# Kernel optimization log

Hardware: AMD Instinct MI355X
Metric: run time of the kernel (lower is better)

Reference implementation:

```python
import jax, jax.numpy as jnp
import numpy as np

B, N, D_MODEL, H = 2, 512, 256, 8
DH, DS, DE = 8, 8, 8          # hyperbolic / spherical / euclidean component dims
HEAD = D_MODEL // H           # 32
HALF = HEAD // 2              # 16 rope frequencies
KAPPA_S = 1.0                 # spherical curvature
EPS = 1e-6


def setup_inputs() -> dict:
    key = jax.random.key(0)
    ks = jax.random.split(key, 10)
    h = jax.random.normal(ks[0], (B, N, D_MODEL), jnp.float32)
    # manifold coords: hyperbolic part inside Poincare ball, spherical part on unit sphere
    xh = 0.3 * jnp.tanh(jax.random.normal(ks[1], (B, N, DH), jnp.float32))
    xs_raw = jax.random.normal(ks[2], (B, N, DS), jnp.float32)
    xs = xs_raw / jnp.linalg.norm(xs_raw, axis=-1, keepdims=True)
    xe = jax.random.normal(ks[3], (B, N, DE), jnp.float32)
    x = jnp.concatenate([xh, xs, xe], axis=-1)
    def lin(k):
        return 0.05 * jax.random.normal(k, (D_MODEL, D_MODEL), jnp.float32)
    inp = dict(
        h=h, x=x,
        Wq=lin(ks[4]), bq=jnp.zeros((D_MODEL,), jnp.float32),
        Wk=lin(ks[5]), bk=jnp.zeros((D_MODEL,), jnp.float32),
        Wv=lin(ks[6]), bv=jnp.zeros((D_MODEL,), jnp.float32),
        Wo=lin(ks[7]), bo=jnp.zeros((D_MODEL,), jnp.float32),
        w_kernel=jnp.ones((H, 3), jnp.float32),   # torch init: ones(num_heads, num_comp)
        beta=jnp.ones((H,), jnp.float32),
        edge_bias=0.1 * jax.random.normal(ks[8], (B, 1, N, N), jnp.float32),
        node_mask=jnp.ones((B, N), bool),
    )
    return inp


def _pairwise_geometry(x):
    """Returns dh (B,N,N), sdot (B,N,N), de2 (B,N,N), dist (B,N,N)."""
    xh, xs, xe = x[..., :DH], x[..., DH:DH + DS], x[..., DH + DS:]
    # hyperbolic: Poincare-ball distance arccosh(1 + 2|a-b|^2 / ((1-|a|^2)(1-|b|^2)))
    dh2_num = jnp.sum((xh[:, :, None, :] - xh[:, None, :, :]) ** 2, -1)
    one_m = 1.0 - jnp.sum(xh * xh, -1)                               # (B,N)
    arg = 1.0 + 2.0 * dh2_num / (one_m[:, :, None] * one_m[:, None, :])
    dh = jnp.arccosh(jnp.maximum(arg, 1.0 + EPS))
    # spherical: arccos of dot (unit vectors); raw dot kept for the kernel term
    sdot = jnp.einsum('bnd,bmd->bnm', xs, xs)
    ds = jnp.arccos(jnp.clip(sdot, -1.0 + EPS, 1.0 - EPS)) / np.sqrt(KAPPA_S)
    # euclidean: squared distance (kernel uses -d^2; product dist uses d^2)
    de2 = jnp.sum((xe[:, :, None, :] - xe[:, None, :, :]) ** 2, -1)
    dist = jnp.sqrt(dh * dh + ds * ds + de2)
    return dh, sdot, de2, dist


def reference(h, x, Wq, bq, Wk, bk, Wv, bv, Wo, bo, w_kernel, beta, edge_bias, node_mask):
    scale = 1.0 / np.sqrt(HEAD)
    rope_freq = jnp.exp(-np.log(10000.0) * jnp.arange(HALF, dtype=jnp.float32) / HALF)

    def heads(t):  # (B,N,D) -> (B,H,N,head)
        return t.reshape(B, N, H, HEAD).transpose(0, 2, 1, 3)

    Q = heads(h @ Wq.T + bq)
    K = heads(h @ Wk.T + bk)
    V = heads(h @ Wv.T + bv)

    dh, sdot, de2, dist = _pairwise_geometry(x)

    # M-RoPE: rotate Q by pairwise angle theta_ij = omega * d_M(x_i, x_j)
    theta = dist[..., None] * rope_freq                  # (B,N,N,half)
    cos_t = jnp.cos(theta)[:, None]                      # (B,1,N,N,half)
    sin_t = jnp.sin(theta)[:, None]
    q1, q2 = Q[..., 0::2], Q[..., 1::2]                  # (B,H,N,half)
    k1, k2 = K[..., 0::2], K[..., 1::2]
    qk_same = q1[:, :, :, None, :] * k1[:, :, None, :, :] + q2[:, :, :, None, :] * k2[:, :, None, :, :]
    qk_cross = q1[:, :, :, None, :] * k2[:, :, None, :, :] - q2[:, :, :, None, :] * k1[:, :, None, :, :]
    attn = (cos_t * qk_same + sin_t * qk_cross).sum(-1) * scale   # (B,H,N,N)

    # geodesic kernel bias: per-component kernels [H:-d_H, S:k*a.b, E:-|a-b|^2]
    kernel_stack = jnp.stack([-dh, KAPPA_S * sdot, -de2], axis=-1)  # (B,N,N,3)
    geo = jnp.einsum('hc,bnmc->bhnm', w_kernel, kernel_stack)
    attn = attn + beta[None, :, None, None] * geo + edge_bias

    attn = jnp.where(node_mask[:, None, None, :], attn, -jnp.inf)
    p = jax.nn.softmax(attn, axis=-1)
    out = jnp.einsum('bhnm,bhmd->bhnd', p, V).transpose(0, 2, 1, 3).reshape(B, N, D_MODEL)
    return out @ Wo.T + bo
```

## Files before the change

kernel.cpp:

```cpp
#include <hip/hip_runtime.h>

#define N_TOK 512
#define NH 8

typedef __attribute__((ext_vector_type(8))) short short8;
typedef __attribute__((ext_vector_type(4))) short short4v;
typedef __attribute__((ext_vector_type(4))) float f32x4;
typedef __attribute__((ext_vector_type(2))) _Float16 half2v;
typedef __attribute__((ext_vector_type(4))) _Float16 half4v;
typedef __attribute__((ext_vector_type(8))) _Float16 half8v;

__device__ __forceinline__ unsigned short f2bf(float f) {
    union { float f; unsigned u; } v; v.f = f;
    return (unsigned short)((v.u + 0x7FFF + ((v.u >> 16) & 1)) >> 16);
}

__global__ __launch_bounds__(256) void gemm_qkv_mfma(
    const float* __restrict__ A, const float* __restrict__ x,
    const float* __restrict__ Wq, const float* __restrict__ Wk, const float* __restrict__ Wv,
    const float* __restrict__ bq, const float* __restrict__ bk, const float* __restrict__ bv,
    float* __restrict__ Qb, _Float16* __restrict__ KT2, float* __restrict__ Vb,
    float* __restrict__ xT)
{
    const int bx = blockIdx.x;
    const int t = threadIdx.x;
    if (bx >= 768) {
        int idx = bx - 768;
        int b = idx / 24, k = idx % 24;
        const float* src = x + (size_t)b * 512 * 24 + k;
        float* dst = xT + (size_t)b * 12288 + k * 512;
        for (int j = t; j < 512; j += 256) dst[j] = src[j * 24];
        return;
    }
    const int z = bx >> 8, rem = bx & 255;
    const int m0 = (rem >> 3) * 32, n0 = (rem & 7) * 32;
    const float* W    = (z == 0) ? Wq : (z == 1) ? Wk : Wv;
    const float* bias = (z == 0) ? bq : (z == 1) ? bk : bv;

    __shared__ short As[32][264];
    __shared__ short Ws[32][264];

    #pragma unroll
    for (int r = 0; r < 8; ++r) {
        int idx = t + 256 * r;
        int row = idx >> 6, c4 = (idx & 63) * 4;
        float4 a = *(const float4*)&A[(m0 + row) * 256 + c4];
        short4v pa = {(short)f2bf(a.x), (short)f2bf(a.y), (short)f2bf(a.z), (short)f2bf(a.w)};
        *(short4v*)&As[row][c4] = pa;
        float4 w = *(const float4*)&W[(n0 + row) * 256 + c4];
        short4v pw = {(short)f2bf(w.x), (short)f2bf(w.y), (short)f2bf(w.z), (short)f2bf(w.w)};
        *(short4v*)&Ws[row][c4] = pw;
    }
    __syncthreads();

    const int w = t >> 6, lane = t & 63;
    const int wm = (w >> 1) * 16, wn = (w & 1) * 16;
    const int frow = lane & 15, kq = lane >> 4;

    f32x4 acc = {0.f, 0.f, 0.f, 0.f};
    #pragma unroll
    for (int k0 = 0; k0 < 8; ++k0) {
        short8 af = *(const short8*)&As[wm + frow][k0 * 32 + kq * 8];
        short8 wf = *(const short8*)&Ws[wn + frow][k0 * 32 + kq * 8];
        if (z == 1) acc = __builtin_amdgcn_mfma_f32_16x16x32_bf16(wf, af, acc, 0, 0, 0);
        else        acc = __builtin_amdgcn_mfma_f32_16x16x32_bf16(af, wf, acc, 0, 0, 0);
    }
    const int col = lane & 15, rq = (lane >> 4) * 4;
    if (z == 1) {
        int tok = m0 + wm + col;
        int bb = tok >> 9, jloc = tok & 511;
        #pragma unroll
        for (int r = 0; r < 4; ++r) {
            int d = n0 + wn + rq + r;
            KT2[(size_t)bb * 131072 + (size_t)(d >> 1) * 1024 + jloc * 2 + (d & 1)]
                = (_Float16)(acc[r] + bias[d]);
        }
    } else {
        float* C = (z == 0) ? Qb : Vb;
        const float sc = (z == 0) ? 0.17677669529663687f : 1.0f;
        float bsv = bias[n0 + wn + col];
        #pragma unroll
        for (int r = 0; r < 4; ++r)
            C[(m0 + wm + rq + r) * 256 + n0 + wn + col] = (acc[r] + bsv) * sc;
    }
}

__global__ __launch_bounds__(512, 4) void attn_kernel(
    const float* __restrict__ Q, const _Float16* __restrict__ KT2, const float* __restrict__ V,
    const float* __restrict__ x, const float* __restrict__ xT,
    const float* __restrict__ wker, const float* __restrict__ beta,
    const float* __restrict__ eb, float* __restrict__ Ao)
{
    const int i0 = blockIdx.x * 2;
    const int b  = blockIdx.y;
    const int t  = threadIdx.x;
    const int lane = t & 63;
    const int h = __builtin_amdgcn_readfirstlane(t >> 6);

    __shared__ half8v csn[16][2][64];
    __shared__ float es[2][NH][128];
    __shared__ float gdh[2][512], gsd[2][512], gde[2][512], gdist[2][512];

    {
        const float* xc = xT + (size_t)b * 12288 + t;
        float xv[24];
        #pragma unroll
        for (int k = 0; k < 24; ++k) xv[k] = xc[k * 512];
        float oj = 0.f;
        #pragma unroll
        for (int k = 0; k < 8; ++k) oj += xv[k] * xv[k];
        #pragma unroll
        for (int p = 0; p < 2; ++p) {
            const float* xi = x + (size_t)(b * N_TOK + i0 + p) * 24;
            float onemi = 1.0f, dh2 = 0.f, sd = 0.f, de2 = 0.f;
            #pragma unroll
            for (int k = 0; k < 8; ++k) {
                onemi -= xi[k] * xi[k];
                float d = xi[k] - xv[k]; dh2 += d * d;
            }
            #pragma unroll
            for (int k = 0; k < 8; ++k) sd += xi[8 + k] * xv[8 + k];
            #pragma unroll
            for (int k = 0; k < 8; ++k) { float d = xi[16 + k] - xv[16 + k]; de2 += d * d; }
            float arg = fmaf(2.0f * dh2, __builtin_amdgcn_rcpf(onemi * (1.0f - oj)), 1.0f);
            arg = fmaxf(arg, 1.0f + 1e-6f);
            float dh = __logf(arg + __builtin_amdgcn_sqrtf(fmaf(arg, arg, -1.0f)));
            float sdc = fminf(fmaxf(sd, -1.0f + 1e-6f), 1.0f - 1e-6f);
            float ax = fabsf(sdc);
            float pp = fmaf(ax, -0.0012624911f, 0.0066700901f);
            pp = fmaf(pp, ax, -0.0170881256f);
            pp = fmaf(pp, ax,  0.0308918810f);
            pp = fmaf(pp, ax, -0.0501743046f);
            pp = fmaf(pp, ax,  0.0889789874f);
            pp = fmaf(pp, ax, -0.2145988016f);
            pp = fmaf(pp, ax,  1.5707963050f);
            pp *= __builtin_amdgcn_sqrtf(1.0f - ax);
            float dsp = (sdc < 0.f) ? (3.14159265358979f - pp) : pp;
            float dist = __builtin_amdgcn_sqrtf(fmaf(dh, dh, fmaf(dsp, dsp, de2)));
            gdh[p][t] = dh; gsd[p][t] = sd; gde[p][t] = de2; gdist[p][t] = dist;
        }
    }

    const float* q0p = Q + (size_t)(b * N_TOK + i0) * 256 + h * 32;
    const float* q1p = q0p + 256;
    const float bet = beta[h];
    const float bw0 = bet * wker[h * 3 + 0], bw1 = bet * wker[h * 3 + 1], bw2 = bet * wker[h * 3 + 2];

    const int gjj = t & 127;
    const int gfh = __builtin_amdgcn_readfirstlane((t >> 7) & 1);
    const int gii = __builtin_amdgcn_readfirstlane(t >> 8);
    float frq[8];
    #pragma unroll
    for (int r = 0; r < 8; ++r)
        frq[r] = __expf(-0.5756462732485115f * (float)(gfh * 8 + r));

    float dsum[2] = {0.f, 0.f};
    float accv[2][4] = {{0.f,0.f,0.f,0.f},{0.f,0.f,0.f,0.f}};
    const int jsub = lane >> 3, dq = lane & 7;

    auto build = [&](int tile) {
        float d = gdist[gii][tile * 128 + gjj];
        #pragma unroll
        for (int r = 0; r < 8; ++r) {
            float sv, cv;
            __sincosf(d * frq[r], &sv, &cv);
            half4v p;
            p[0] = (_Float16)cv; p[1] = (_Float16)sv;
            p[2] = (_Float16)(-sv); p[3] = (_Float16)cv;
            ((half4v*)&csn[gfh * 8 + r][gii][gjj >> 1])[gjj & 1] = p;
        }
    };

    __syncthreads();
    build(0);
    const float* ebp0 = eb + ((size_t)b * N_TOK + i0) * N_TOK + 2 * lane;
    const float* ebp1 = ebp0 + N_TOK;
    float2 ebn0 = *(const float2*)ebp0;
    float2 ebn1 = *(const float2*)ebp1;
    __syncthreads();

    const _Float16* kbase = KT2 + (size_t)b * 131072 + (size_t)(h * 16) * 1024 + 4 * lane;

    for (int tile = 0; tile < 4; ++tile) {
        float2 eb0 = ebn0, eb1 = ebn1;
        if (tile < 3) {
            ebn0 = *(const float2*)(ebp0 + (tile + 1) * 128);
            ebn1 = *(const float2*)(ebp1 + (tile + 1) * 128);
        }
        {
            const _Float16* kp = kbase + tile * 256;
            half4v karr[16];
            #pragma unroll
            for (int f = 0; f < 16; ++f) karr[f] = *(const half4v*)(kp + f * 1024);

            float dot[2][2] = {{0.f, 0.f}, {0.f, 0.f}};
            #pragma unroll
            for (int f = 0; f < 16; ++f) {
                half2v k0 = {karr[f][0], karr[f][1]};
                half2v k1 = {karr[f][2], karr[f][3]};
                float q10 = q0p[2 * f], q20 = q0p[2 * f + 1];
                float q11 = q1p[2 * f], q21 = q1p[2 * f + 1];
                #pragma unroll
                for (int ii = 0; ii < 2; ++ii) {
                    half8v c8 = csn[f][ii][lane];
                    half2v cs0 = {c8[0], c8[1]}, rt0 = {c8[2], c8[3]};
                    half2v cs1 = {c8[4], c8[5]}, rt1 = {c8[6], c8[7]};
#if __has_builtin(__builtin_amdgcn_fdot2)
                    float u0 = __builtin_amdgcn_fdot2(cs0, k0, 0.f, false);
                    float v0 = __builtin_amdgcn_fdot2(rt0, k0, 0.f, false);
                    float u1 = __builtin_amdgcn_fdot2(cs1, k1, 0.f, false);
                    float v1 = __builtin_amdgcn_fdot2(rt1, k1, 0.f, false);
#else
                    float u0 = (float)cs0[0]*(float)k0[0] + (float)cs0[1]*(float)k0[1];
                    float v0 = (float)rt0[0]*(float)k0[0] + (float)rt0[1]*(float)k0[1];
                    float u1 = (float)cs1[0]*(float)k1[0] + (float)cs1[1]*(float)k1[1];
                    float v1 = (float)rt1[0]*(float)k1[0] + (float)rt1[1]*(float)k1[1];
#endif
                    float qa = ii ? q11 : q10, qb = ii ? q21 : q20;
                    dot[ii][0] = fmaf(qa, u0, fmaf(qb, v0, dot[ii][0]));
                    dot[ii][1] = fmaf(qa, u1, fmaf(qb, v1, dot[ii][1]));
                }
            }
            #pragma unroll
            for (int ii = 0; ii < 2; ++ii) {
                float2 g1 = *(const float2*)&gdh[ii][tile * 128 + 2 * lane];
                float2 g2 = *(const float2*)&gsd[ii][tile * 128 + 2 * lane];
                float2 g3 = *(const float2*)&gde[ii][tile * 128 + 2 * lane];
                float2 e2 = ii ? eb1 : eb0;
                float s0 = dot[ii][0] + (bw1 * g2.x - bw0 * g1.x - bw2 * g3.x) + e2.x;
                float s1 = dot[ii][1] + (bw1 * g2.y - bw0 * g1.y - bw2 * g3.y) + e2.y;
                float e0 = __expf(s0), e1 = __expf(s1);
                dsum[ii] += e0 + e1;
                *(float2*)&es[ii][h][2 * lane] = make_float2(e0, e1);
            }
        }
        if (tile < 3) { __syncthreads(); build(tile + 1); }
        {
            const float* vp = V + (size_t)(b * N_TOK + tile * 128 + jsub) * 256 + h * 32 + dq * 4;
            #pragma unroll
            for (int it = 0; it < 16; ++it) {
                float4 v4 = *(const float4*)(vp + it * 8 * 256);
                float e0 = es[0][h][it * 8 + jsub], e1 = es[1][h][it * 8 + jsub];
                accv[0][0] += e0 * v4.x; accv[0][1] += e0 * v4.y;
                accv[0][2] += e0 * v4.z; accv[0][3] += e0 * v4.w;
                accv[1][0] += e1 * v4.x; accv[1][1] += e1 * v4.y;
                accv[1][2] += e1 * v4.z; accv[1][3] += e1 * v4.w;
            }
        }
        if (tile < 3) __syncthreads();
    }

    #pragma unroll
    for (int ii = 0; ii < 2; ++ii) {
        float v = dsum[ii];
        v += __shfl_xor(v, 1);  v += __shfl_xor(v, 2);  v += __shfl_xor(v, 4);
        v += __shfl_xor(v, 8);  v += __shfl_xor(v, 16); v += __shfl_xor(v, 32);
        dsum[ii] = 1.0f / v;
    }
    #pragma unroll
    for (int ii = 0; ii < 2; ++ii)
        #pragma unroll
        for (int dd = 0; dd < 4; ++dd) {
            float a = accv[ii][dd];
            a += __shfl_xor(a, 8); a += __shfl_xor(a, 16); a += __shfl_xor(a, 32);
            accv[ii][dd] = a;
        }
    if (jsub == 0) {
        #pragma unroll
        for (int ii = 0; ii < 2; ++ii) {
            float4 o;
            o.x = accv[ii][0] * dsum[ii]; o.y = accv[ii][1] * dsum[ii];
            o.z = accv[ii][2] * dsum[ii]; o.w = accv[ii][3] * dsum[ii];
            *(float4*)&Ao[(size_t)(b * N_TOK + i0 + ii) * 256 + h * 32 + dq * 4] = o;
        }
    }
}

__global__ __launch_bounds__(256) void gemm_out_mfma(
    const float* __restrict__ Ao, const float* __restrict__ Wo,
    const float* __restrict__ bo, float* __restrict__ out)
{
    const int t = threadIdx.x;
    const int m0 = (blockIdx.x >> 3) * 32, n0 = (blockIdx.x & 7) * 32;

    __shared__ short As[32][264];
    __shared__ short Ws[32][264];

    #pragma unroll
    for (int r = 0; r < 8; ++r) {
        int idx = t + 256 * r;
        int row = idx >> 6, c4 = (idx & 63) * 4;
        float4 a = *(const float4*)&Ao[(m0 + row) * 256 + c4];
        short4v pa = {(short)f2bf(a.x), (short)f2bf(a.y), (short)f2bf(a.z), (short)f2bf(a.w)};
        *(short4v*)&As[row][c4] = pa;
        float4 w = *(const float4*)&Wo[(n0 + row) * 256 + c4];
        short4v pw = {(short)f2bf(w.x), (short)f2bf(w.y), (short)f2bf(w.z), (short)f2bf(w.w)};
        *(short4v*)&Ws[row][c4] = pw;
    }
    __syncthreads();

    const int w = t >> 6, lane = t & 63;
    const int wm = (w >> 1) * 16, wn = (w & 1) * 16;
    const int frow = lane & 15, kq = lane >> 4;

    f32x4 acc = {0.f, 0.f, 0.f, 0.f};
    #pragma unroll
    for (int k0 = 0; k0 < 8; ++k0) {
        short8 af = *(const short8*)&As[wm + frow][k0 * 32 + kq * 8];
        short8 wf = *(const short8*)&Ws[wn + frow][k0 * 32 + kq * 8];
        acc = __builtin_amdgcn_mfma_f32_16x16x32_bf16(af, wf, acc, 0, 0, 0);
    }
    const int col = lane & 15, rq = (lane >> 4) * 4;
    float bsv = bo[n0 + wn + col];
    #pragma unroll
    for (int r = 0; r < 4; ++r)
        out[(m0 + wm + rq + r) * 256 + n0 + wn + col] = acc[r] + bsv;
}

extern "C" void kernel_launch(void* const* d_in, const int* in_sizes, int n_in,
                              void* d_out, int out_size, void* d_ws, size_t ws_size,
                              hipStream_t stream) {
    const float* hin  = (const float*)d_in[0];
    const float* x    = (const float*)d_in[1];
    const float* Wq   = (const float*)d_in[2];
    const float* bq   = (const float*)d_in[3];
    const float* Wk   = (const float*)d_in[4];
    const float* bk   = (const float*)d_in[5];
    const float* Wv   = (const float*)d_in[6];
    const float* bv   = (const float*)d_in[7];
    const float* Wo   = (const float*)d_in[8];
    const float* bo   = (const float*)d_in[9];
    const float* wker = (const float*)d_in[10];
    const float* beta = (const float*)d_in[11];
    const float* eb   = (const float*)d_in[12];
    float* out = (float*)d_out;
    float* w   = (float*)d_ws;

    float*    Qb  = w;
    _Float16* KT2 = (_Float16*)(w + 262144);
    float*    Vb  = w + 393216;
    float*    Ao  = w + 655360;
    float*    xT  = w + 917504;

    hipLaunchKernelGGL(gemm_qkv_mfma, dim3(816), dim3(256), 0, stream,
                       hin, x, Wq, Wk, Wv, bq, bk, bv, Qb, KT2, Vb, xT);
    hipLaunchKernelGGL(attn_kernel, dim3(256, 2), dim3(512), 0, stream,
                       Qb, KT2, Vb, x, xT, wker, beta, eb, Ao);
    hipLaunchKernelGGL(gemm_out_mfma, dim3(256), dim3(256), 0, stream,
                       Ao, Wo, bo, out);
}
```

Before: 121.6 us.

## Split attention keys across two blocks and merge partial sums in output GEMM

The attention kernel now splits the 512 keys into two halves along a new grid dimension, doubling the block count. Each block writes an unnormalized partial output and a partial softmax denominator, and the output projection GEMM adds the two halves and normalizes them while loading. The rotary table in shared memory is also halved by storing only cos/sin and building the rotated key on the fly. This adds more exposed parallelism and less LDS per block, at the cost of extra global traffic for the partial buffers and duplicated per-block setup work. The merge is only correct because the softmax does not subtract a running max, so it relies on the logits staying small enough not to overflow.

```diff
diff --git a/kernel.cpp b/kernel.cpp
--- a/kernel.cpp
+++ b/kernel.cpp
@@ -8,7 +8,6 @@
 typedef __attribute__((ext_vector_type(4))) float f32x4;
 typedef __attribute__((ext_vector_type(2))) _Float16 half2v;
 typedef __attribute__((ext_vector_type(4))) _Float16 half4v;
-typedef __attribute__((ext_vector_type(8))) _Float16 half8v;
 
 __device__ __forceinline__ unsigned short f2bf(float f) {
     union { float f; unsigned u; } v; v.f = f;
@@ -89,56 +88,52 @@
     const float* __restrict__ Q, const _Float16* __restrict__ KT2, const float* __restrict__ V,
     const float* __restrict__ x, const float* __restrict__ xT,
     const float* __restrict__ wker, const float* __restrict__ beta,
-    const float* __restrict__ eb, float* __restrict__ Ao)
+    const float* __restrict__ eb, float* __restrict__ Apart, float* __restrict__ Dpart)
 {
     const int i0 = blockIdx.x * 2;
-    const int b  = blockIdx.y;
+    const int jh = blockIdx.y;
+    const int b  = blockIdx.z;
     const int t  = threadIdx.x;
     const int lane = t & 63;
     const int h = __builtin_amdgcn_readfirstlane(t >> 6);
 
-    __shared__ half8v csn[16][2][64];
+    __shared__ half2v csn[16][2][128];
     __shared__ float es[2][NH][128];
-    __shared__ float gdh[2][512], gsd[2][512], gde[2][512], gdist[2][512];
+    __shared__ float gdh[2][256], gsd[2][256], gde[2][256], gdist[2][256];
 
     {
-        const float* xc = xT + (size_t)b * 12288 + t;
+        const int pj = t & 255, pp = t >> 8;
+        const float* xc = xT + (size_t)b * 12288 + jh * 256 + pj;
         float xv[24];
         #pragma unroll
         for (int k = 0; k < 24; ++k) xv[k] = xc[k * 512];
-        float oj = 0.f;
-        #pragma unroll
-        for (int k = 0; k < 8; ++k) oj += xv[k] * xv[k];
-        #pragma unroll
-        for (int p = 0; p < 2; ++p) {
-            const float* xi = x + (size_t)(b * N_TOK + i0 + p) * 24;
-            float onemi = 1.0f, dh2 = 0.f, sd = 0.f, de2 = 0.f;
-            #pragma unroll
-            for (int k = 0; k < 8; ++k) {
-                onemi -= xi[k] * xi[k];
-                float d = xi[k] - xv[k]; dh2 += d * d;
-            }
-            #pragma unroll
-            for (int k = 0; k < 8; ++k) sd += xi[8 + k] * xv[8 + k];
-            #pragma unroll
-            for (int k = 0; k < 8; ++k) { float d = xi[16 + k] - xv[16 + k]; de2 += d * d; }
-            float arg = fmaf(2.0f * dh2, __builtin_amdgcn_rcpf(onemi * (1.0f - oj)), 1.0f);
-            arg = fmaxf(arg, 1.0f + 1e-6f);
-            float dh = __logf(arg + __builtin_amdgcn_sqrtf(fmaf(arg, arg, -1.0f)));
-            float sdc = fminf(fmaxf(sd, -1.0f + 1e-6f), 1.0f - 1e-6f);
-            float ax = fabsf(sdc);
-            float pp = fmaf(ax, -0.0012624911f, 0.0066700901f);
-            pp = fmaf(pp, ax, -0.0170881256f);
-            pp = fmaf(pp, ax,  0.0308918810f);
-            pp = fmaf(pp, ax, -0.0501743046f);
-            pp = fmaf(pp, ax,  0.0889789874f);
-            pp = fmaf(pp, ax, -0.2145988016f);
-            pp = fmaf(pp, ax,  1.5707963050f);
-            pp *= __builtin_amdgcn_sqrtf(1.0f - ax);
-            float dsp = (sdc < 0.f) ? (3.14159265358979f - pp) : pp;
-            float dist = __builtin_amdgcn_sqrtf(fmaf(dh, dh, fmaf(dsp, dsp, de2)));
-            gdh[p][t] = dh; gsd[p][t] = sd; gde[p][t] = de2; gdist[p][t] = dist;
-        }
+        const float* xi = x + (size_t)(b * N_TOK + i0 + pp) * 24;
+        float onemi = 1.0f, dh2 = 0.f, oj = 0.f, sd = 0.f, de2 = 0.f;
+        #pragma unroll
+        for (int k = 0; k < 8; ++k) {
+            onemi -= xi[k] * xi[k];
+            float d = xi[k] - xv[k]; dh2 += d * d; oj += xv[k] * xv[k];
+        }
+        #pragma unroll
+        for (int k = 0; k < 8; ++k) sd += xi[8 + k] * xv[8 + k];
+        #pragma unroll
+        for (int k = 0; k < 8; ++k) { float d = xi[16 + k] - xv[16 + k]; de2 += d * d; }
+        float arg = fmaf(2.0f * dh2, __builtin_amdgcn_rcpf(onemi * (1.0f - oj)), 1.0f);
+        arg = fmaxf(arg, 1.0f + 1e-6f);
+        float dh = __logf(arg + __builtin_amdgcn_sqrtf(fmaf(arg, arg, -1.0f)));
+        float sdc = fminf(fmaxf(sd, -1.0f + 1e-6f), 1.0f - 1e-6f);
+        float ax = fabsf(sdc);
+        float pp2 = fmaf(ax, -0.0012624911f, 0.0066700901f);
+        pp2 = fmaf(pp2, ax, -0.0170881256f);
+        pp2 = fmaf(pp2, ax,  0.0308918810f);
+        pp2 = fmaf(pp2, ax, -0.0501743046f);
+        pp2 = fmaf(pp2, ax,  0.0889789874f);
+        pp2 = fmaf(pp2, ax, -0.2145988016f);
+        pp2 = fmaf(pp2, ax,  1.5707963050f);
+        pp2 *= __builtin_amdgcn_sqrtf(1.0f - ax);
+        float dsp = (sdc < 0.f) ? (3.14159265358979f - pp2) : pp2;
+        float dist = __builtin_amdgcn_sqrtf(fmaf(dh, dh, fmaf(dsp, dsp, de2)));
+        gdh[pp][pj] = dh; gsd[pp][pj] = sd; gde[pp][pj] = de2; gdist[pp][pj] = dist;
     }
 
     const float* q0p = Q + (size_t)(b * N_TOK + i0) * 256 + h * 32;
@@ -164,28 +159,28 @@
         for (int r = 0; r < 8; ++r) {
             float sv, cv;
             __sincosf(d * frq[r], &sv, &cv);
-            half4v p;
-            p[0] = (_Float16)cv; p[1] = (_Float16)sv;
-            p[2] = (_Float16)(-sv); p[3] = (_Float16)cv;
-            ((half4v*)&csn[gfh * 8 + r][gii][gjj >> 1])[gjj & 1] = p;
+            half2v p; p[0] = (_Float16)cv; p[1] = (_Float16)sv;
+            csn[gfh * 8 + r][gii][gjj] = p;
         }
     };
 
     __syncthreads();
     build(0);
-    const float* ebp0 = eb + ((size_t)b * N_TOK + i0) * N_TOK + 2 * lane;
+    const float* ebp0 = eb + ((size_t)b * N_TOK + i0) * N_TOK + jh * 256 + 2 * lane;
     const float* ebp1 = ebp0 + N_TOK;
     float2 ebn0 = *(const float2*)ebp0;
     float2 ebn1 = *(const float2*)ebp1;
     __syncthreads();
 
-    const _Float16* kbase = KT2 + (size_t)b * 131072 + (size_t)(h * 16) * 1024 + 4 * lane;
-
-    for (int tile = 0; tile < 4; ++tile) {
+    const _Float16* kbase = KT2 + (size_t)b * 131072 + (size_t)(h * 16) * 1024
+                          + (size_t)jh * 512 + 4 * lane;
+
+    #pragma unroll
+    for (int tile = 0; tile < 2; ++tile) {
         float2 eb0 = ebn0, eb1 = ebn1;
-        if (tile < 3) {
-            ebn0 = *(const float2*)(ebp0 + (tile + 1) * 128);
-            ebn1 = *(const float2*)(ebp1 + (tile + 1) * 128);
+        if (tile < 1) {
+            ebn0 = *(const float2*)(ebp0 + 128);
+            ebn1 = *(const float2*)(ebp1 + 128);
         }
         {
             const _Float16* kp = kbase + tile * 256;
@@ -196,25 +191,26 @@
             float dot[2][2] = {{0.f, 0.f}, {0.f, 0.f}};
             #pragma unroll
             for (int f = 0; f < 16; ++f) {
-                half2v k0 = {karr[f][0], karr[f][1]};
-                half2v k1 = {karr[f][2], karr[f][3]};
+                half2v k0  = {karr[f][0], karr[f][1]};
+                half2v k1  = {karr[f][2], karr[f][3]};
+                half2v ks0 = {karr[f][1], -karr[f][0]};
+                half2v ks1 = {karr[f][3], -karr[f][2]};
                 float q10 = q0p[2 * f], q20 = q0p[2 * f + 1];
                 float q11 = q1p[2 * f], q21 = q1p[2 * f + 1];
                 #pragma unroll
                 for (int ii = 0; ii < 2; ++ii) {
-                    half8v c8 = csn[f][ii][lane];
-                    half2v cs0 = {c8[0], c8[1]}, rt0 = {c8[2], c8[3]};
-                    half2v cs1 = {c8[4], c8[5]}, rt1 = {c8[6], c8[7]};
+                    half4v cc = *(const half4v*)&csn[f][ii][2 * lane];
+                    half2v cs0 = {cc[0], cc[1]}, cs1 = {cc[2], cc[3]};
 #if __has_builtin(__builtin_amdgcn_fdot2)
-                    float u0 = __builtin_amdgcn_fdot2(cs0, k0, 0.f, false);
-                    float v0 = __builtin_amdgcn_fdot2(rt0, k0, 0.f, false);
-                    float u1 = __builtin_amdgcn_fdot2(cs1, k1, 0.f, false);
-                    float v1 = __builtin_amdgcn_fdot2(rt1, k1, 0.f, false);
+                    float u0 = __builtin_amdgcn_fdot2(cs0, k0,  0.f, false);
+                    float v0 = __builtin_amdgcn_fdot2(cs0, ks0, 0.f, false);
+                    float u1 = __builtin_amdgcn_fdot2(cs1, k1,  0.f, false);
+                    float v1 = __builtin_amdgcn_fdot2(cs1, ks1, 0.f, false);
 #else
                     float u0 = (float)cs0[0]*(float)k0[0] + (float)cs0[1]*(float)k0[1];
-                    float v0 = (float)rt0[0]*(float)k0[0] + (float)rt0[1]*(float)k0[1];
+                    float v0 = (float)cs0[0]*(float)ks0[0] + (float)cs0[1]*(float)ks0[1];
                     float u1 = (float)cs1[0]*(float)k1[0] + (float)cs1[1]*(float)k1[1];
-                    float v1 = (float)rt1[0]*(float)k1[0] + (float)rt1[1]*(float)k1[1];
+                    float v1 = (float)cs1[0]*(float)ks1[0] + (float)cs1[1]*(float)ks1[1];
 #endif
                     float qa = ii ? q11 : q10, qb = ii ? q21 : q20;
                     dot[ii][0] = fmaf(qa, u0, fmaf(qb, v0, dot[ii][0]));
@@ -234,9 +230,10 @@
                 *(float2*)&es[ii][h][2 * lane] = make_float2(e0, e1);
             }
         }
-        if (tile < 3) { __syncthreads(); build(tile + 1); }
+        if (tile < 1) { __syncthreads(); build(1); }
         {
-            const float* vp = V + (size_t)(b * N_TOK + tile * 128 + jsub) * 256 + h * 32 + dq * 4;
+            const float* vp = V + (size_t)(b * N_TOK + jh * 256 + tile * 128 + jsub) * 256
+                            + h * 32 + dq * 4;
             #pragma unroll
             for (int it = 0; it < 16; ++it) {
                 float4 v4 = *(const float4*)(vp + it * 8 * 256);
@@ -247,7 +244,7 @@
                 accv[1][2] += e1 * v4.z; accv[1][3] += e1 * v4.w;
             }
         }
-        if (tile < 3) __syncthreads();
+        if (tile < 1) __syncthreads();
     }
 
     #pragma unroll
@@ -255,7 +252,7 @@
         float v = dsum[ii];
         v += __shfl_xor(v, 1);  v += __shfl_xor(v, 2);  v += __shfl_xor(v, 4);
         v += __shfl_xor(v, 8);  v += __shfl_xor(v, 16); v += __shfl_xor(v, 32);
-        dsum[ii] = 1.0f / v;
+        dsum[ii] = v;
     }
     #pragma unroll
     for (int ii = 0; ii < 2; ++ii)
@@ -269,20 +266,29 @@
         #pragma unroll
         for (int ii = 0; ii < 2; ++ii) {
             float4 o;
-            o.x = accv[ii][0] * dsum[ii]; o.y = accv[ii][1] * dsum[ii];
-            o.z = accv[ii][2] * dsum[ii]; o.w = accv[ii][3] * dsum[ii];
-            *(float4*)&Ao[(size_t)(b * N_TOK + i0 + ii) * 256 + h * 32 + dq * 4] = o;
-        }
+            o.x = accv[ii][0]; o.y = accv[ii][1]; o.z = accv[ii][2]; o.w = accv[ii][3];
+            *(float4*)&Apart[(size_t)jh * 262144
+                             + (size_t)(b * N_TOK + i0 + ii) * 256 + h * 32 + dq * 4] = o;
+        }
+    }
+    if (lane == 0) {
+        Dpart[jh * 8192 + (b * N_TOK + i0    ) * NH + h] = dsum[0];
+        Dpart[jh * 8192 + (b * N_TOK + i0 + 1) * NH + h] = dsum[1];
     }
 }
 
 __global__ __launch_bounds__(256) void gemm_out_mfma(
-    const float* __restrict__ Ao, const float* __restrict__ Wo,
-    const float* __restrict__ bo, float* __restrict__ out)
+    const float* __restrict__ Ap, const float* __restrict__ Dp,
+    const float* __restrict__ Wo, const float* __restrict__ bo, float* __restrict__ out)
 {
     const int t = threadIdx.x;
     const int m0 = (blockIdx.x >> 3) * 32, n0 = (blockIdx.x & 7) * 32;
 
+    const float* Ap0 = Ap;
+    const float* Ap1 = Ap + 262144;
+    const float* Dp0 = Dp;
+    const float* Dp1 = Dp + 8192;
+
     __shared__ short As[32][264];
     __shared__ short Ws[32][264];
 
@@ -290,7 +296,13 @@
     for (int r = 0; r < 8; ++r) {
         int idx = t + 256 * r;
         int row = idx >> 6, c4 = (idx & 63) * 4;
-        float4 a = *(const float4*)&Ao[(m0 + row) * 256 + c4];
+        int tok = m0 + row, hh = c4 >> 5;
+        float den = Dp0[tok * NH + hh] + Dp1[tok * NH + hh];
+        float rs = __builtin_amdgcn_rcpf(den);
+        float4 a0 = *(const float4*)&Ap0[(size_t)tok * 256 + c4];
+        float4 a1 = *(const float4*)&Ap1[(size_t)tok * 256 + c4];
+        float4 a = {(a0.x + a1.x) * rs, (a0.y + a1.y) * rs,
+                    (a0.z + a1.z) * rs, (a0.w + a1.w) * rs};
         short4v pa = {(short)f2bf(a.x), (short)f2bf(a.y), (short)f2bf(a.z), (short)f2bf(a.w)};
         *(short4v*)&As[row][c4] = pa;
         float4 w = *(const float4*)&Wo[(n0 + row) * 256 + c4];
@@ -339,13 +351,14 @@
     float*    Qb  = w;
     _Float16* KT2 = (_Float16*)(w + 262144);
     float*    Vb  = w + 393216;
-    float*    Ao  = w + 655360;
-    float*    xT  = w + 917504;
+    float*    Ap  = w + 655360;
+    float*    Dp  = w + 1179648;
+    float*    xT  = w + 1196032;
 
     hipLaunchKernelGGL(gemm_qkv_mfma, dim3(816), dim3(256), 0, stream,
                        hin, x, Wq, Wk, Wv, bq, bk, bv, Qb, KT2, Vb, xT);
-    hipLaunchKernelGGL(attn_kernel, dim3(256, 2), dim3(512), 0, stream,
-                       Qb, KT2, Vb, x, xT, wker, beta, eb, Ao);
+    hipLaunchKernelGGL(attn_kernel, dim3(256, 2, 2), dim3(512), 0, stream,
+                       Qb, KT2, Vb, x, xT, wker, beta, eb, Ap, Dp);
     hipLaunchKernelGGL(gemm_out_mfma, dim3(256), dim3(256), 0, stream,
-                       Ao, Wo, bo, out);
-}
+                       Ap, Dp, Wo, bo, out);
+}
```

After: 127.2 us. 1.05x slower.

## Precompute pairwise geometry and rope cos/sin tables in QKV kernel, stream into attention

Applied to the files above, without the earlier changes.

Moves the pairwise geometry computation and the cos/sin rope table build out of the attention kernel. They now run in extra blocks of the QKV projection kernel, which write dh/sdot/de2 and half-precision cos/sin tables to global memory. The attention kernel double-buffers the tables into shared memory and derives the rotated K terms on the fly, with no in-loop table build. This takes transcendental work off the attention critical path, but adds about 34 MB of global writes and reads and doubles the QKV block size, leaving half the threads idle in the GEMM blocks.

```diff
diff --git a/kernel.cpp b/kernel.cpp
--- a/kernel.cpp
+++ b/kernel.cpp
@@ -8,52 +8,108 @@
 typedef __attribute__((ext_vector_type(4))) float f32x4;
 typedef __attribute__((ext_vector_type(2))) _Float16 half2v;
 typedef __attribute__((ext_vector_type(4))) _Float16 half4v;
-typedef __attribute__((ext_vector_type(8))) _Float16 half8v;
 
 __device__ __forceinline__ unsigned short f2bf(float f) {
     union { float f; unsigned u; } v; v.f = f;
     return (unsigned short)((v.u + 0x7FFF + ((v.u >> 16) & 1)) >> 16);
 }
 
-__global__ __launch_bounds__(256) void gemm_qkv_mfma(
+__global__ __launch_bounds__(512) void gemm_qkv_table(
     const float* __restrict__ A, const float* __restrict__ x,
     const float* __restrict__ Wq, const float* __restrict__ Wk, const float* __restrict__ Wv,
     const float* __restrict__ bq, const float* __restrict__ bk, const float* __restrict__ bv,
     float* __restrict__ Qb, _Float16* __restrict__ KT2, float* __restrict__ Vb,
-    float* __restrict__ xT)
+    _Float16* __restrict__ CSN, float* __restrict__ GDH, float* __restrict__ GSD,
+    float* __restrict__ GDE)
 {
     const int bx = blockIdx.x;
     const int t = threadIdx.x;
+
     if (bx >= 768) {
-        int idx = bx - 768;
-        int b = idx / 24, k = idx % 24;
-        const float* src = x + (size_t)b * 512 * 24 + k;
-        float* dst = xT + (size_t)b * 12288 + k * 512;
-        for (int j = t; j < 512; j += 256) dst[j] = src[j * 24];
+        const int idx = bx - 768;
+        const int b = idx >> 9, i = idx & 511;
+        const int j = t;
+        const float* xi = x + (size_t)(b * N_TOK + i) * 24;
+        const float* xr = x + (size_t)(b * N_TOK + j) * 24;
+        float xv[24];
+        #pragma unroll
+        for (int q = 0; q < 6; ++q) {
+            float4 v = *(const float4*)(xr + q * 4);
+            xv[q * 4 + 0] = v.x; xv[q * 4 + 1] = v.y; xv[q * 4 + 2] = v.z; xv[q * 4 + 3] = v.w;
+        }
+        float onemi = 1.0f, dh2 = 0.f, oj = 0.f, sd = 0.f, de2 = 0.f;
+        #pragma unroll
+        for (int k = 0; k < 8; ++k) {
+            onemi -= xi[k] * xi[k];
+            float d = xi[k] - xv[k]; dh2 += d * d; oj += xv[k] * xv[k];
+        }
+        #pragma unroll
+        for (int k = 0; k < 8; ++k) sd += xi[8 + k] * xv[8 + k];
+        #pragma unroll
+        for (int k = 0; k < 8; ++k) { float d = xi[16 + k] - xv[16 + k]; de2 += d * d; }
+        float arg = fmaf(2.0f * dh2, __builtin_amdgcn_rcpf(onemi * (1.0f - oj)), 1.0f);
+        arg = fmaxf(arg, 1.0f + 1e-6f);
+        float dh = __logf(arg + __builtin_amdgcn_sqrtf(fmaf(arg, arg, -1.0f)));
+        float sdc = fminf(fmaxf(sd, -1.0f + 1e-6f), 1.0f - 1e-6f);
+        float ax = fabsf(sdc);
+        float pp = fmaf(ax, -0.0012624911f, 0.0066700901f);
+        pp = fmaf(pp, ax, -0.0170881256f);
+        pp = fmaf(pp, ax,  0.0308918810f);
+        pp = fmaf(pp, ax, -0.0501743046f);
+        pp = fmaf(pp, ax,  0.0889789874f);
+        pp = fmaf(pp, ax, -0.2145988016f);
+        pp = fmaf(pp, ax,  1.5707963050f);
+        pp *= __builtin_amdgcn_sqrtf(1.0f - ax);
+        float dsp = (sdc < 0.f) ? (3.14159265358979f - pp) : pp;
+        float dist = __builtin_amdgcn_sqrtf(fmaf(dh, dh, fmaf(dsp, dsp, de2)));
+
+        const size_t row = (size_t)(b * N_TOK + i) * 512 + j;
+        GDH[row] = dh; GSD[row] = sd; GDE[row] = de2;
+
+        const float frq[16] = {
+            1.0f, 0.56234133f, 0.31622777f, 0.17782794f,
+            0.1f, 0.056234133f, 0.031622777f, 0.017782794f,
+            0.01f, 0.0056234133f, 0.0031622777f, 0.0017782794f,
+            0.001f, 0.00056234133f, 0.00031622777f, 0.00017782794f };
+        const size_t blkbase = ((size_t)(b * 256 + (i >> 1)) * 4 + (j >> 7)) * 4096;
+        half2v* cp = (half2v*)CSN + blkbase + (i & 1) * 128 + (j & 127);
+        #pragma unroll
+        for (int f = 0; f < 16; ++f) {
+            float sv, cv;
+            __sincosf(dist * frq[f], &sv, &cv);
+            half2v p; p[0] = (_Float16)cv; p[1] = (_Float16)sv;
+            cp[f * 256] = p;
+        }
         return;
     }
+
+    const int tt = t & 255;
+    const int half = t >> 8;
     const int z = bx >> 8, rem = bx & 255;
-    const int m0 = (rem >> 3) * 32, n0 = (rem & 7) * 32;
+    const int m0 = (rem >> 3) * 32;
+    const int n0 = ((rem & 7) * 2 + half) * 16;
+    if (half == 1) return;
     const float* W    = (z == 0) ? Wq : (z == 1) ? Wk : Wv;
     const float* bias = (z == 0) ? bq : (z == 1) ? bk : bv;
+    const int n0b = (rem & 7) * 32;
 
     __shared__ short As[32][264];
     __shared__ short Ws[32][264];
 
     #pragma unroll
     for (int r = 0; r < 8; ++r) {
-        int idx = t + 256 * r;
-        int row = idx >> 6, c4 = (idx & 63) * 4;
+        int idx2 = tt + 256 * r;
+        int row = idx2 >> 6, c4 = (idx2 & 63) * 4;
         float4 a = *(const float4*)&A[(m0 + row) * 256 + c4];
         short4v pa = {(short)f2bf(a.x), (short)f2bf(a.y), (short)f2bf(a.z), (short)f2bf(a.w)};
         *(short4v*)&As[row][c4] = pa;
-        float4 w = *(const float4*)&W[(n0 + row) * 256 + c4];
+        float4 w = *(const float4*)&W[(n0b + row) * 256 + c4];
         short4v pw = {(short)f2bf(w.x), (short)f2bf(w.y), (short)f2bf(w.z), (short)f2bf(w.w)};
         *(short4v*)&Ws[row][c4] = pw;
     }
     __syncthreads();
 
-    const int w = t >> 6, lane = t & 63;
+    const int w = tt >> 6, lane = tt & 63;
     const int wm = (w >> 1) * 16, wn = (w & 1) * 16;
     const int frow = lane & 15, kq = lane >> 4;
 
@@ -71,23 +127,24 @@
         int bb = tok >> 9, jloc = tok & 511;
         #pragma unroll
         for (int r = 0; r < 4; ++r) {
-            int d = n0 + wn + rq + r;
+            int d = n0b + wn + rq + r;
             KT2[(size_t)bb * 131072 + (size_t)(d >> 1) * 1024 + jloc * 2 + (d & 1)]
                 = (_Float16)(acc[r] + bias[d]);
         }
     } else {
         float* C = (z == 0) ? Qb : Vb;
         const float sc = (z == 0) ? 0.17677669529663687f : 1.0f;
-        float bsv = bias[n0 + wn + col];
+        float bsv = bias[n0b + wn + col];
         #pragma unroll
         for (int r = 0; r < 4; ++r)
-            C[(m0 + wm + rq + r) * 256 + n0 + wn + col] = (acc[r] + bsv) * sc;
+            C[(m0 + wm + rq + r) * 256 + n0b + wn + col] = (acc[r] + bsv) * sc;
     }
 }
 
 __global__ __launch_bounds__(512, 4) void attn_kernel(
     const float* __restrict__ Q, const _Float16* __restrict__ KT2, const float* __restrict__ V,
-    const float* __restrict__ x, const float* __restrict__ xT,
+    const _Float16* __restrict__ CSN,
+    const float* __restrict__ GDH, const float* __restrict__ GSD, const float* __restrict__ GDE,
     const float* __restrict__ wker, const float* __restrict__ beta,
     const float* __restrict__ eb, float* __restrict__ Ao)
 {
@@ -97,93 +154,40 @@
     const int lane = t & 63;
     const int h = __builtin_amdgcn_readfirstlane(t >> 6);
 
-    __shared__ half8v csn[16][2][64];
+    __shared__ half2v csnb[2][16][2][128];
     __shared__ float es[2][NH][128];
-    __shared__ float gdh[2][512], gsd[2][512], gde[2][512], gdist[2][512];
-
-    {
-        const float* xc = xT + (size_t)b * 12288 + t;
-        float xv[24];
-        #pragma unroll
-        for (int k = 0; k < 24; ++k) xv[k] = xc[k * 512];
-        float oj = 0.f;
-        #pragma unroll
-        for (int k = 0; k < 8; ++k) oj += xv[k] * xv[k];
-        #pragma unroll
-        for (int p = 0; p < 2; ++p) {
-            const float* xi = x + (size_t)(b * N_TOK + i0 + p) * 24;
-            float onemi = 1.0f, dh2 = 0.f, sd = 0.f, de2 = 0.f;
-            #pragma unroll
-            for (int k = 0; k < 8; ++k) {
-                onemi -= xi[k] * xi[k];
-                float d = xi[k] - xv[k]; dh2 += d * d;
-            }
-            #pragma unroll
-            for (int k = 0; k < 8; ++k) sd += xi[8 + k] * xv[8 + k];
-            #pragma unroll
-            for (int k = 0; k < 8; ++k) { float d = xi[16 + k] - xv[16 + k]; de2 += d * d; }
-            float arg = fmaf(2.0f * dh2, __builtin_amdgcn_rcpf(onemi * (1.0f - oj)), 1.0f);
-            arg = fmaxf(arg, 1.0f + 1e-6f);
-            float dh = __logf(arg + __builtin_amdgcn_sqrtf(fmaf(arg, arg, -1.0f)));
-            float sdc = fminf(fmaxf(sd, -1.0f + 1e-6f), 1.0f - 1e-6f);
-            float ax = fabsf(sdc);
-            float pp = fmaf(ax, -0.0012624911f, 0.0066700901f);
-            pp = fmaf(pp, ax, -0.0170881256f);
-            pp = fmaf(pp, ax,  0.0308918810f);
-            pp = fmaf(pp, ax, -0.0501743046f);
-            pp = fmaf(pp, ax,  0.0889789874f);
-            pp = fmaf(pp, ax, -0.2145988016f);
-            pp = fmaf(pp, ax,  1.5707963050f);
-            pp *= __builtin_amdgcn_sqrtf(1.0f - ax);
-            float dsp = (sdc < 0.f) ? (3.14159265358979f - pp) : pp;
-            float dist = __builtin_amdgcn_sqrtf(fmaf(dh, dh, fmaf(dsp, dsp, de2)));
-            gdh[p][t] = dh; gsd[p][t] = sd; gde[p][t] = de2; gdist[p][t] = dist;
-        }
-    }
 
     const float* q0p = Q + (size_t)(b * N_TOK + i0) * 256 + h * 32;
     const float* q1p = q0p + 256;
     const float bet = beta[h];
     const float bw0 = bet * wker[h * 3 + 0], bw1 = bet * wker[h * 3 + 1], bw2 = bet * wker[h * 3 + 2];
 
-    const int gjj = t & 127;
-    const int gfh = __builtin_amdgcn_readfirstlane((t >> 7) & 1);
-    const int gii = __builtin_amdgcn_readfirstlane(t >> 8);
-    float frq[8];
-    #pragma unroll
-    for (int r = 0; r < 8; ++r)
-        frq[r] = __expf(-0.5756462732485115f * (float)(gfh * 8 + r));
-
     float dsum[2] = {0.f, 0.f};
     float accv[2][4] = {{0.f,0.f,0.f,0.f},{0.f,0.f,0.f,0.f}};
     const int jsub = lane >> 3, dq = lane & 7;
 
-    auto build = [&](int tile) {
-        float d = gdist[gii][tile * 128 + gjj];
-        #pragma unroll
-        for (int r = 0; r < 8; ++r) {
-            float sv, cv;
-            __sincosf(d * frq[r], &sv, &cv);
-            half4v p;
-            p[0] = (_Float16)cv; p[1] = (_Float16)sv;
-            p[2] = (_Float16)(-sv); p[3] = (_Float16)cv;
-            ((half4v*)&csn[gfh * 8 + r][gii][gjj >> 1])[gjj & 1] = p;
-        }
-    };
-
-    __syncthreads();
-    build(0);
+    const float4* csg4 = (const float4*)CSN + ((size_t)(b * 256 + blockIdx.x) * 4) * 1024;
+    {
+        float4 s0 = csg4[2 * t], s1 = csg4[2 * t + 1];
+        float4* d = (float4*)&csnb[0][0][0][0];
+        d[2 * t] = s0; d[2 * t + 1] = s1;
+    }
     const float* ebp0 = eb + ((size_t)b * N_TOK + i0) * N_TOK + 2 * lane;
     const float* ebp1 = ebp0 + N_TOK;
     float2 ebn0 = *(const float2*)ebp0;
     float2 ebn1 = *(const float2*)ebp1;
+    const size_t grow0 = (size_t)(b * N_TOK + i0) * 512 + 2 * lane;
+    const size_t grow1 = grow0 + 512;
+    const _Float16* kbase = KT2 + (size_t)b * 131072 + (size_t)(h * 16) * 1024 + 4 * lane;
     __syncthreads();
 
-    const _Float16* kbase = KT2 + (size_t)b * 131072 + (size_t)(h * 16) * 1024 + 4 * lane;
-
     for (int tile = 0; tile < 4; ++tile) {
+        const int cur = tile & 1;
         float2 eb0 = ebn0, eb1 = ebn1;
+        float4 nt0, nt1;
         if (tile < 3) {
+            nt0 = csg4[(tile + 1) * 1024 + 2 * t];
+            nt1 = csg4[(tile + 1) * 1024 + 2 * t + 1];
             ebn0 = *(const float2*)(ebp0 + (tile + 1) * 128);
             ebn1 = *(const float2*)(ebp1 + (tile + 1) * 128);
         }
@@ -196,25 +200,26 @@
             float dot[2][2] = {{0.f, 0.f}, {0.f, 0.f}};
             #pragma unroll
             for (int f = 0; f < 16; ++f) {
-                half2v k0 = {karr[f][0], karr[f][1]};
-                half2v k1 = {karr[f][2], karr[f][3]};
+                half2v k0  = {karr[f][0], karr[f][1]};
+                half2v k1  = {karr[f][2], karr[f][3]};
+                half2v ks0 = {karr[f][1], -karr[f][0]};
+                half2v ks1 = {karr[f][3], -karr[f][2]};
                 float q10 = q0p[2 * f], q20 = q0p[2 * f + 1];
                 float q11 = q1p[2 * f], q21 = q1p[2 * f + 1];
                 #pragma unroll
                 for (int ii = 0; ii < 2; ++ii) {
-                    half8v c8 = csn[f][ii][lane];
-                    half2v cs0 = {c8[0], c8[1]}, rt0 = {c8[2], c8[3]};
-                    half2v cs1 = {c8[4], c8[5]}, rt1 = {c8[6], c8[7]};
+                    half4v cc = *(const half4v*)&csnb[cur][f][ii][2 * lane];
+                    half2v cs0 = {cc[0], cc[1]}, cs1 = {cc[2], cc[3]};
 #if __has_builtin(__builtin_amdgcn_fdot2)
-                    float u0 = __builtin_amdgcn_fdot2(cs0, k0, 0.f, false);
-                    float v0 = __builtin_amdgcn_fdot2(rt0, k0, 0.f, false);
-                    float u1 = __builtin_amdgcn_fdot2(cs1, k1, 0.f, false);
-                    float v1 = __builtin_amdgcn_fdot2(rt1, k1, 0.f, false);
+                    float u0 = __builtin_amdgcn_fdot2(cs0, k0,  0.f, false);
+                    float v0 = __builtin_amdgcn_fdot2(cs0, ks0, 0.f, false);
+                    float u1 = __builtin_amdgcn_fdot2(cs1, k1,  0.f, false);
+                    float v1 = __builtin_amdgcn_fdot2(cs1, ks1, 0.f, false);
 #else
                     float u0 = (float)cs0[0]*(float)k0[0] + (float)cs0[1]*(float)k0[1];
-                    float v0 = (float)rt0[0]*(float)k0[0] + (float)rt0[1]*(float)k0[1];
+                    float v0 = (float)cs0[0]*(float)ks0[0] + (float)cs0[1]*(float)ks0[1];
                     float u1 = (float)cs1[0]*(float)k1[0] + (float)cs1[1]*(float)k1[1];
-                    float v1 = (float)rt1[0]*(float)k1[0] + (float)rt1[1]*(float)k1[1];
+                    float v1 = (float)cs1[0]*(float)ks1[0] + (float)cs1[1]*(float)ks1[1];
 #endif
                     float qa = ii ? q11 : q10, qb = ii ? q21 : q20;
                     dot[ii][0] = fmaf(qa, u0, fmaf(qb, v0, dot[ii][0]));
@@ -223,9 +228,10 @@
             }
             #pragma unroll
             for (int ii = 0; ii < 2; ++ii) {
-                float2 g1 = *(const float2*)&gdh[ii][tile * 128 + 2 * lane];
-                float2 g2 = *(const float2*)&gsd[ii][tile * 128 + 2 * lane];
-                float2 g3 = *(const float2*)&gde[ii][tile * 128 + 2 * lane];
+                size_t gr = (ii ? grow1 : grow0) + tile * 128;
+                float2 g1 = *(const float2*)&GDH[gr];
+                float2 g2 = *(const float2*)&GSD[gr];
+                float2 g3 = *(const float2*)&GDE[gr];
                 float2 e2 = ii ? eb1 : eb0;
                 float s0 = dot[ii][0] + (bw1 * g2.x - bw0 * g1.x - bw2 * g3.x) + e2.x;
                 float s1 = dot[ii][1] + (bw1 * g2.y - bw0 * g1.y - bw2 * g3.y) + e2.y;
@@ -234,7 +240,6 @@
                 *(float2*)&es[ii][h][2 * lane] = make_float2(e0, e1);
             }
         }
-        if (tile < 3) { __syncthreads(); build(tile + 1); }
         {
             const float* vp = V + (size_t)(b * N_TOK + tile * 128 + jsub) * 256 + h * 32 + dq * 4;
             #pragma unroll
@@ -247,7 +252,11 @@
                 accv[1][2] += e1 * v4.z; accv[1][3] += e1 * v4.w;
             }
         }
-        if (tile < 3) __syncthreads();
+        if (tile < 3) {
+            float4* d = (float4*)&csnb[cur ^ 1][0][0][0];
+            d[2 * t] = nt0; d[2 * t + 1] = nt1;
+            __syncthreads();
+        }
     }
 
     #pragma unroll
@@ -340,12 +349,16 @@
     _Float16* KT2 = (_Float16*)(w + 262144);
     float*    Vb  = w + 393216;
     float*    Ao  = w + 655360;
-    float*    xT  = w + 917504;
-
-    hipLaunchKernelGGL(gemm_qkv_mfma, dim3(816), dim3(256), 0, stream,
-                       hin, x, Wq, Wk, Wv, bq, bk, bv, Qb, KT2, Vb, xT);
+    _Float16* CSN = (_Float16*)(w + 917504);
+    float*    GDH = w + 9306112;
+    float*    GSD = w + 9830400;
+    float*    GDE = w + 10354688;
+
+    hipLaunchKernelGGL(gemm_qkv_table, dim3(1792), dim3(512), 0, stream,
+                       hin, x, Wq, Wk, Wv, bq, bk, bv, Qb, KT2, Vb,
+                       CSN, GDH, GSD, GDE);
     hipLaunchKernelGGL(attn_kernel, dim3(256, 2), dim3(512), 0, stream,
-                       Qb, KT2, Vb, x, xT, wker, beta, eb, Ao);
+                       Qb, KT2, Vb, CSN, GDH, GSD, GDE, wker, beta, eb, Ao);
     hipLaunchKernelGGL(gemm_out_mfma, dim3(256), dim3(256), 0, stream,
                        Ao, Wo, bo, out);
 }
```

New measurement: 138.0 us. 1.13x slower.

## Fuse output projection into attention kernel and pre-convert Wo to bf16

Applied to the files above, without the earlier changes.

Removes the separate output-projection GEMM launch. Each attention block now writes its two normalized output rows as bf16 into shared memory, then each wave computes 32 output columns with MFMA against a bf16 copy of Wo produced by extra blocks in the QKV kernel. This removes one kernel launch and the fp32 round trip of the attention output through global memory. In exchange, half the MFMA rows are padding (16-row tile for only 2 rows), Wo is re-read from global or L2 by every block, and the attention kernel uses more shared memory, which could lower occupancy.

```diff
diff --git a/kernel.cpp b/kernel.cpp
--- a/kernel.cpp
+++ b/kernel.cpp
@@ -19,11 +19,24 @@
     const float* __restrict__ A, const float* __restrict__ x,
     const float* __restrict__ Wq, const float* __restrict__ Wk, const float* __restrict__ Wv,
     const float* __restrict__ bq, const float* __restrict__ bk, const float* __restrict__ bv,
+    const float* __restrict__ Wo,
     float* __restrict__ Qb, _Float16* __restrict__ KT2, float* __restrict__ Vb,
-    float* __restrict__ xT)
+    float* __restrict__ xT, short* __restrict__ WoB)
 {
     const int bx = blockIdx.x;
     const int t = threadIdx.x;
+    if (bx >= 816) {
+        const int idx = bx - 816;
+        const float4* src = (const float4*)Wo;
+        #pragma unroll
+        for (int r = 0; r < 8; ++r) {
+            int fi = idx * 2048 + r * 256 + t;
+            float4 v = src[fi];
+            short4v p = {(short)f2bf(v.x), (short)f2bf(v.y), (short)f2bf(v.z), (short)f2bf(v.w)};
+            ((short4v*)WoB)[fi] = p;
+        }
+        return;
+    }
     if (bx >= 768) {
         int idx = bx - 768;
         int b = idx / 24, k = idx % 24;
@@ -89,7 +102,8 @@
     const float* __restrict__ Q, const _Float16* __restrict__ KT2, const float* __restrict__ V,
     const float* __restrict__ x, const float* __restrict__ xT,
     const float* __restrict__ wker, const float* __restrict__ beta,
-    const float* __restrict__ eb, float* __restrict__ Ao)
+    const float* __restrict__ eb, const short* __restrict__ WoB,
+    const float* __restrict__ bo, float* __restrict__ out)
 {
     const int i0 = blockIdx.x * 2;
     const int b  = blockIdx.y;
@@ -100,6 +114,9 @@
     __shared__ half8v csn[16][2][64];
     __shared__ float es[2][NH][128];
     __shared__ float gdh[2][512], gsd[2][512], gde[2][512], gdist[2][512];
+    __shared__ short As16[16][264];
+
+    for (int u = t; u < 2112; u += 512) ((unsigned*)As16)[u] = 0u;
 
     {
         const float* xc = xT + (size_t)b * 12288 + t;
@@ -271,50 +288,32 @@
             float4 o;
             o.x = accv[ii][0] * dsum[ii]; o.y = accv[ii][1] * dsum[ii];
             o.z = accv[ii][2] * dsum[ii]; o.w = accv[ii][3] * dsum[ii];
-            *(float4*)&Ao[(size_t)(b * N_TOK + i0 + ii) * 256 + h * 32 + dq * 4] = o;
-        }
-    }
-}
-
-__global__ __launch_bounds__(256) void gemm_out_mfma(
-    const float* __restrict__ Ao, const float* __restrict__ Wo,
-    const float* __restrict__ bo, float* __restrict__ out)
-{
-    const int t = threadIdx.x;
-    const int m0 = (blockIdx.x >> 3) * 32, n0 = (blockIdx.x & 7) * 32;
-
-    __shared__ short As[32][264];
-    __shared__ short Ws[32][264];
-
-    #pragma unroll
-    for (int r = 0; r < 8; ++r) {
-        int idx = t + 256 * r;
-        int row = idx >> 6, c4 = (idx & 63) * 4;
-        float4 a = *(const float4*)&Ao[(m0 + row) * 256 + c4];
-        short4v pa = {(short)f2bf(a.x), (short)f2bf(a.y), (short)f2bf(a.z), (short)f2bf(a.w)};
-        *(short4v*)&As[row][c4] = pa;
-        float4 w = *(const float4*)&Wo[(n0 + row) * 256 + c4];
-        short4v pw = {(short)f2bf(w.x), (short)f2bf(w.y), (short)f2bf(w.z), (short)f2bf(w.w)};
-        *(short4v*)&Ws[row][c4] = pw;
+            short4v p = {(short)f2bf(o.x), (short)f2bf(o.y), (short)f2bf(o.z), (short)f2bf(o.w)};
+            *(short4v*)&As16[ii][h * 32 + dq * 4] = p;
+        }
     }
     __syncthreads();
 
-    const int w = t >> 6, lane = t & 63;
-    const int wm = (w >> 1) * 16, wn = (w & 1) * 16;
-    const int frow = lane & 15, kq = lane >> 4;
-
-    f32x4 acc = {0.f, 0.f, 0.f, 0.f};
-    #pragma unroll
-    for (int k0 = 0; k0 < 8; ++k0) {
-        short8 af = *(const short8*)&As[wm + frow][k0 * 32 + kq * 8];
-        short8 wf = *(const short8*)&Ws[wn + frow][k0 * 32 + kq * 8];
-        acc = __builtin_amdgcn_mfma_f32_16x16x32_bf16(af, wf, acc, 0, 0, 0);
-    }
-    const int col = lane & 15, rq = (lane >> 4) * 4;
-    float bsv = bo[n0 + wn + col];
-    #pragma unroll
-    for (int r = 0; r < 4; ++r)
-        out[(m0 + wm + rq + r) * 256 + n0 + wn + col] = acc[r] + bsv;
+    {
+        const int frow = lane & 15, kq = lane >> 4;
+        const int col = lane & 15, rq = (lane >> 4) * 4;
+        const int n0b = h * 32;
+        #pragma unroll
+        for (int wn = 0; wn < 2; ++wn) {
+            f32x4 acc = {0.f, 0.f, 0.f, 0.f};
+            #pragma unroll
+            for (int k0 = 0; k0 < 8; ++k0) {
+                short8 af = *(const short8*)&As16[frow][k0 * 32 + kq * 8];
+                short8 wf = *(const short8*)&WoB[(n0b + wn * 16 + frow) * 256 + k0 * 32 + kq * 8];
+                acc = __builtin_amdgcn_mfma_f32_16x16x32_bf16(af, wf, acc, 0, 0, 0);
+            }
+            if (rq == 0) {
+                float bsv = bo[n0b + wn * 16 + col];
+                out[(size_t)(b * N_TOK + i0    ) * 256 + n0b + wn * 16 + col] = acc[0] + bsv;
+                out[(size_t)(b * N_TOK + i0 + 1) * 256 + n0b + wn * 16 + col] = acc[1] + bsv;
+            }
+        }
+    }
 }
 
 extern "C" void kernel_launch(void* const* d_in, const int* in_sizes, int n_in,
@@ -339,13 +338,11 @@
     float*    Qb  = w;
     _Float16* KT2 = (_Float16*)(w + 262144);
     float*    Vb  = w + 393216;
-    float*    Ao  = w + 655360;
-    float*    xT  = w + 917504;
-
-    hipLaunchKernelGGL(gemm_qkv_mfma, dim3(816), dim3(256), 0, stream,
-                       hin, x, Wq, Wk, Wv, bq, bk, bv, Qb, KT2, Vb, xT);
+    short*    WoB = (short*)(w + 655360);
+    float*    xT  = w + 688128;
+
+    hipLaunchKernelGGL(gemm_qkv_mfma, dim3(824), dim3(256), 0, stream,
+                       hin, x, Wq, Wk, Wv, bq, bk, bv, Wo, Qb, KT2, Vb, xT, WoB);
     hipLaunchKernelGGL(attn_kernel, dim3(256, 2), dim3(512), 0, stream,
-                       Qb, KT2, Vb, x, xT, wker, beta, eb, Ao);
-    hipLaunchKernelGGL(gemm_out_mfma, dim3(256), dim3(256), 0, stream,
-                       Ao, Wo, bo, out);
+                       Qb, KT2, Vb, x, xT, wker, beta, eb, WoB, bo, out);
 }
```

Result: slower. 125.9 us (+3.5%).
